# Kernel tuning notes

Measured on AMD Instinct MI355X. Metric: run time of the kernel, lower is better.

Reference implementation:

```python
import jax, jax.numpy as jnp
import numpy as np
import math

VOCAB = 32000
D = 1024
SEQ = 2048
BATCH = 4
PAD_IDX = 0
LN_EPS = 1e-5


def make_sinusoidal_pe(max_len, d):
    position = jnp.arange(max_len, dtype=jnp.float32)[:, None]
    div_term = jnp.exp(jnp.arange(0, d, 2, dtype=jnp.float32) * (-math.log(10000.0) / d))
    ang = position * div_term  # [max_len, d/2]
    pe = jnp.zeros((max_len, d), dtype=jnp.float32)
    pe = pe.at[:, 0::2].set(jnp.sin(ang))
    pe = pe.at[:, 1::2].set(jnp.cos(ang))
    return pe


def verse_weights(verse_positions):
    # weight = 1.2 at the first token of each nonzero-verse run (zeros are skipped
    # and do not reset the run), else 1.0. Vectorized via forward-fill of the
    # last nonzero verse id strictly before each position.
    v = verse_positions  # [B, S] int
    S = v.shape[1]
    idx = jnp.where(v != 0, jnp.arange(S)[None, :], -1)
    last_idx = jax.lax.cummax(idx, axis=1)
    prev_idx = jnp.concatenate([jnp.full_like(last_idx[:, :1], -1), last_idx[:, :-1]], axis=1)
    prev_verse = jnp.take_along_axis(v, jnp.clip(prev_idx, 0, None), axis=1)
    prev_verse = jnp.where(prev_idx >= 0, prev_verse, -1)
    return jnp.where((v != 0) & (v != prev_verse), 1.2, 1.0).astype(jnp.float32)


def setup_inputs() -> dict:
    key = jax.random.key(0)
    k1, k2, k3, k4, k5, k6, k7 = jax.random.split(key, 7)
    token_ids = jax.random.randint(k1, (BATCH, SEQ), 0, VOCAB)
    verse_positions = jnp.sort(jax.random.randint(k2, (BATCH, SEQ), 0, 200), axis=-1)
    book_types = jax.random.randint(k3, (BATCH, SEQ), 0, 4)
    # Xavier-uniform embedding table with padding row zeroed
    limit = math.sqrt(6.0 / (VOCAB + D))
    emb_table = jax.random.uniform(k4, (VOCAB, D), jnp.float32, -limit, limit)
    emb_table = emb_table.at[PAD_IDX].set(0.0)
    book_table = jax.random.normal(k5, (4, D), jnp.float32)
    ln_gamma = jnp.ones((D,), jnp.float32)
    ln_beta = jnp.zeros((D,), jnp.float32)
    return {
        "token_ids": token_ids,
        "verse_positions": verse_positions,
        "book_types": book_types,
        "emb_table": emb_table,
        "book_table": book_table,
        "ln_gamma": ln_gamma,
        "ln_beta": ln_beta,
    }


def reference(token_ids, verse_positions, book_types, emb_table, book_table, ln_gamma, ln_beta):
    # Token embedding * sqrt(d)
    x = emb_table[token_ids] * jnp.asarray(math.sqrt(D), jnp.float32)  # [B,S,D]
    # Verse-weighted sinusoidal positional encoding (dropout = identity, eval mode)
    pe = make_sinusoidal_pe(SEQ, D)[None, :, :]  # [1,S,D]
    w = verse_weights(verse_positions)  # [B,S]
    x = x + pe * w[:, :, None]
    # Book-type embedding
    x = x + book_table[book_types]
    # LayerNorm
    mu = jnp.mean(x, axis=-1, keepdims=True)
    var = jnp.mean(jnp.square(x - mu), axis=-1, keepdims=True)
    x = (x - mu) * jax.lax.rsqrt(var + LN_EPS) * ln_gamma + ln_beta
    return x
```

## Files before the change

### kernel.cpp

```cpp
#include <hip/hip_runtime.h>

#define VOCAB 32000
#define DIM   1024
#define SEQ_  2048
#define NBAT  4

__global__ __launch_bounds__(256) void verse_embed_ln_kernel(
    const int*   __restrict__ token_ids,
    const int*   __restrict__ verse_pos,
    const int*   __restrict__ book_types,
    const float* __restrict__ emb_table,
    const float* __restrict__ book_table,
    const float* __restrict__ gamma,
    const float* __restrict__ beta,
    float*       __restrict__ out)
{
    const int row = blockIdx.x;
    const int s   = row & (SEQ_ - 1);
    const int tid = threadIdx.x;
    const int d0  = tid << 2;

    const int tok   = token_ids[row];
    const int bt    = book_types[row];
    const int v     = verse_pos[row];
    const int vprev = (s == 0) ? -1 : verse_pos[row - 1];
    const float w = (v != 0 && v != vprev) ? 1.2f : 1.0f;

    const float4 e  = *reinterpret_cast<const float4*>(emb_table + (size_t)tok * DIM + d0);
    const float4 bk = *reinterpret_cast<const float4*>(book_table + (size_t)bt * DIM + d0);

    const float C2 = -13.287712379549449f / 1024.0f;
    const float sf = (float)s;
    const float f0 = exp2f(C2 * (float)d0);
    const float f1 = exp2f(C2 * (float)(d0 + 2));
    float s0, c0, s1, c1;
    __sincosf(sf * f0, &s0, &c0);
    __sincosf(sf * f1, &s1, &c1);

    const float SQD = 32.0f;
    const float x0 = e.x * SQD + s0 * w + bk.x;
    const float x1 = e.y * SQD + c0 * w + bk.y;
    const float x2 = e.z * SQD + s1 * w + bk.z;
    const float x3 = e.w * SQD + c1 * w + bk.w;

    float sum = x0 + x1 + x2 + x3;
    float sq  = x0 * x0 + x1 * x1 + x2 * x2 + x3 * x3;
    #pragma unroll
    for (int off = 32; off >= 1; off >>= 1) {
        sum += __shfl_xor(sum, off, 64);
        sq  += __shfl_xor(sq,  off, 64);
    }
    __shared__ float lsum[4], lsq[4];
    const int wid = tid >> 6;
    if ((tid & 63) == 0) { lsum[wid] = sum; lsq[wid] = sq; }
    __syncthreads();
    const float tsum = lsum[0] + lsum[1] + lsum[2] + lsum[3];
    const float tsq  = lsq[0]  + lsq[1]  + lsq[2]  + lsq[3];

    const float mean = tsum * (1.0f / (float)DIM);
    const float var  = tsq * (1.0f / (float)DIM) - mean * mean;
    const float rstd = rsqrtf(var + 1e-5f);

    const float4 g  = *reinterpret_cast<const float4*>(gamma + d0);
    const float4 bb = *reinterpret_cast<const float4*>(beta + d0);

    float4 o;
    o.x = (x0 - mean) * rstd * g.x + bb.x;
    o.y = (x1 - mean) * rstd * g.y + bb.y;
    o.z = (x2 - mean) * rstd * g.z + bb.z;
    o.w = (x3 - mean) * rstd * g.w + bb.w;
    *reinterpret_cast<float4*>(out + (size_t)row * DIM + d0) = o;
}

extern "C" void kernel_launch(void* const* d_in, const int* in_sizes, int n_in,
                              void* d_out, int out_size, void* d_ws, size_t ws_size,
                              hipStream_t stream) {
    const int*   token_ids  = (const int*)d_in[0];
    const int*   verse_pos  = (const int*)d_in[1];
    const int*   book_types = (const int*)d_in[2];
    const float* emb_table  = (const float*)d_in[3];
    const float* book_table = (const float*)d_in[4];
    const float* ln_gamma   = (const float*)d_in[5];
    const float* ln_beta    = (const float*)d_in[6];
    float* out = (float*)d_out;

    dim3 grid(NBAT * SEQ_);
    dim3 block(256);
    verse_embed_ln_kernel<<<grid, block, 0, stream>>>(
        token_ids, verse_pos, book_types, emb_table, book_table,
        ln_gamma, ln_beta, out);
}
```

Measured before the change: 17.06 us.

## Map one wavefront per row to drop block-level LayerNorm reduction

```diff
diff --git a/kernel.cpp b/kernel.cpp
--- a/kernel.cpp
+++ b/kernel.cpp
@@ -15,10 +15,10 @@
     const float* __restrict__ beta,
     float*       __restrict__ out)
 {
-    const int row = blockIdx.x;
-    const int s   = row & (SEQ_ - 1);
-    const int tid = threadIdx.x;
-    const int d0  = tid << 2;
+    const int wid  = threadIdx.x >> 6;
+    const int lane = threadIdx.x & 63;
+    const int row  = (blockIdx.x << 2) + wid;
+    const int s    = row & (SEQ_ - 1);
 
     const int tok   = token_ids[row];
     const int bt    = book_types[row];
@@ -26,50 +26,63 @@
     const int vprev = (s == 0) ? -1 : verse_pos[row - 1];
     const float w = (v != 0 && v != vprev) ? 1.2f : 1.0f;
 
-    const float4 e  = *reinterpret_cast<const float4*>(emb_table + (size_t)tok * DIM + d0);
-    const float4 bk = *reinterpret_cast<const float4*>(book_table + (size_t)bt * DIM + d0);
+    const float* __restrict__ erow = emb_table  + (size_t)tok * DIM;
+    const float* __restrict__ brow = book_table + (size_t)bt  * DIM;
 
-    const float C2 = -13.287712379549449f / 1024.0f;
-    const float sf = (float)s;
-    const float f0 = exp2f(C2 * (float)d0);
-    const float f1 = exp2f(C2 * (float)(d0 + 2));
-    float s0, c0, s1, c1;
-    __sincosf(sf * f0, &s0, &c0);
-    __sincosf(sf * f1, &s1, &c1);
+    float4 e[4], bk[4];
+    #pragma unroll
+    for (int c = 0; c < 4; ++c) {
+        const int d0 = (c << 8) + (lane << 2);
+        e[c]  = *reinterpret_cast<const float4*>(erow + d0);
+        bk[c] = *reinterpret_cast<const float4*>(brow + d0);
+    }
 
+    const float C2  = -13.287712379549449f / 1024.0f;
+    const float sf  = (float)s;
     const float SQD = 32.0f;
-    const float x0 = e.x * SQD + s0 * w + bk.x;
-    const float x1 = e.y * SQD + c0 * w + bk.y;
-    const float x2 = e.z * SQD + s1 * w + bk.z;
-    const float x3 = e.w * SQD + c1 * w + bk.w;
 
-    float sum = x0 + x1 + x2 + x3;
-    float sq  = x0 * x0 + x1 * x1 + x2 * x2 + x3 * x3;
+    float x[16];
+    float sum = 0.0f, sq = 0.0f;
+    #pragma unroll
+    for (int c = 0; c < 4; ++c) {
+        const int d0 = (c << 8) + (lane << 2);
+        const float f0 = exp2f(C2 * (float)d0);
+        const float f1 = exp2f(C2 * (float)(d0 + 2));
+        float s0, c0, s1, c1;
+        __sincosf(sf * f0, &s0, &c0);
+        __sincosf(sf * f1, &s1, &c1);
+        const float x0 = e[c].x * SQD + s0 * w + bk[c].x;
+        const float x1 = e[c].y * SQD + c0 * w + bk[c].y;
+        const float x2 = e[c].z * SQD + s1 * w + bk[c].z;
+        const float x3 = e[c].w * SQD + c1 * w + bk[c].w;
+        x[4 * c + 0] = x0; x[4 * c + 1] = x1; x[4 * c + 2] = x2; x[4 * c + 3] = x3;
+        sum += (x0 + x1) + (x2 + x3);
+        sq  += (x0 * x0 + x1 * x1) + (x2 * x2 + x3 * x3);
+    }
+
     #pragma unroll
     for (int off = 32; off >= 1; off >>= 1) {
         sum += __shfl_xor(sum, off, 64);
         sq  += __shfl_xor(sq,  off, 64);
     }
-    __shared__ float lsum[4], lsq[4];
-    const int wid = tid >> 6;
-    if ((tid & 63) == 0) { lsum[wid] = sum; lsq[wid] = sq; }
-    __syncthreads();
-    const float tsum = lsum[0] + lsum[1] + lsum[2] + lsum[3];
-    const float tsq  = lsq[0]  + lsq[1]  + lsq[2]  + lsq[3];
 
-    const float mean = tsum * (1.0f / (float)DIM);
-    const float var  = tsq * (1.0f / (float)DIM) - mean * mean;
+    const float mean = sum * (1.0f / (float)DIM);
+    const float var  = sq * (1.0f / (float)DIM) - mean * mean;
     const float rstd = rsqrtf(var + 1e-5f);
 
-    const float4 g  = *reinterpret_cast<const float4*>(gamma + d0);
-    const float4 bb = *reinterpret_cast<const float4*>(beta + d0);
-
-    float4 o;
-    o.x = (x0 - mean) * rstd * g.x + bb.x;
-    o.y = (x1 - mean) * rstd * g.y + bb.y;
-    o.z = (x2 - mean) * rstd * g.z + bb.z;
-    o.w = (x3 - mean) * rstd * g.w + bb.w;
-    *reinterpret_cast<float4*>(out + (size_t)row * DIM + d0) = o;
+    float* __restrict__ orow = out + (size_t)row * DIM;
+    #pragma unroll
+    for (int c = 0; c < 4; ++c) {
+        const int d0 = (c << 8) + (lane << 2);
+        const float4 g  = *reinterpret_cast<const float4*>(gamma + d0);
+        const float4 bb = *reinterpret_cast<const float4*>(beta  + d0);
+        float4 o;
+        o.x = (x[4 * c + 0] - mean) * rstd * g.x + bb.x;
+        o.y = (x[4 * c + 1] - mean) * rstd * g.y + bb.y;
+        o.z = (x[4 * c + 2] - mean) * rstd * g.z + bb.z;
+        o.w = (x[4 * c + 3] - mean) * rstd * g.w + bb.w;
+        *reinterpret_cast<float4*>(orow + d0) = o;
+    }
 }
 
 extern "C" void kernel_launch(void* const* d_in, const int* in_sizes, int n_in,
@@ -84,7 +97,7 @@
     const float* ln_beta    = (const float*)d_in[6];
     float* out = (float*)d_out;
 
-    dim3 grid(NBAT * SEQ_);
+    dim3 grid((NBAT * SEQ_) / 4);
     dim3 block(256);
     verse_embed_ln_kernel<<<grid, block, 0, stream>>>(
         token_ids, verse_pos, book_types, emb_table, book_table,
```

Result: faster. 16.51 us (-3.2%).
